# Performance work log

Hardware: AMD Instinct MI355X
Metric: run time of the kernel (lower is better)

The kernel has to match this reference:

```python
import jax, jax.numpy as jnp
import numpy as np

B, M, C, S, SD, K, H = 32, 448, 384, 512, 128, 8, 8
DH = C // H
EPS = 1e-5
NEG_SLOPE = 0.2


def setup_inputs() -> dict:
    key = jax.random.key(0)
    ks = iter(jax.random.split(key, 32))
    nrm = lambda shape, scale=0.05: (jax.random.normal(next(ks), shape, jnp.float32) * scale)
    inp = {
        'q': jax.random.normal(next(ks), (B, M, C), jnp.float32),
        'coarse': jax.random.normal(next(ks), (B, M, 3), jnp.float32),
        'skeleton': jax.random.normal(next(ks), (B, S, 3), jnp.float32),
        # GraphConv 1: 3 -> 64 (root weight, rel/neighbor weight, bias)
        'gc1_wroot': nrm((3, 64), 0.3), 'gc1_wrel': nrm((3, 64), 0.3), 'gc1_b': jnp.zeros((64,), jnp.float32),
        # GraphConv 2: 64 -> SD
        'gc2_wroot': nrm((64, SD), 0.1), 'gc2_wrel': nrm((64, SD), 0.1), 'gc2_b': jnp.zeros((SD,), jnp.float32),
        # skeleton_projection: SD -> C
        'proj_w': nrm((SD, C), 0.08), 'proj_b': jnp.zeros((C,), jnp.float32),
        # MultiheadAttention (torch layout: in_proj (3C, C), out_proj (C, C))
        'attn_in_w': nrm((3 * C, C), 0.05), 'attn_in_b': jnp.zeros((3 * C,), jnp.float32),
        'attn_out_w': nrm((C, C), 0.05), 'attn_out_b': jnp.zeros((C,), jnp.float32),
        # increase_dim: Conv1d(C,1024,1) + BN(1024) + LeakyReLU + Conv1d(1024,1024,1)
        'inc1_w': nrm((1024, C), 0.05), 'inc1_b': jnp.zeros((1024,), jnp.float32),
        'bn_g': jnp.ones((1024,), jnp.float32), 'bn_b': jnp.zeros((1024,), jnp.float32),
        'bn_m': jnp.zeros((1024,), jnp.float32), 'bn_v': jnp.ones((1024,), jnp.float32),
        'inc2_w': nrm((1024, 1024), 0.03), 'inc2_b': jnp.zeros((1024,), jnp.float32),
        # reduce_map: Linear(C + 1024 + 3, C)
        'red_w': nrm((1024 + C + 3, C), 0.03), 'red_b': jnp.zeros((C,), jnp.float32),
    }
    return inp


def _knn_idx(pts):
    # pts: [B,S,3]; per-batch kNN (self excluded), matching knn_graph(k=K, batch=...)
    d2 = jnp.sum((pts[:, :, None, :] - pts[:, None, :, :]) ** 2, axis=-1)  # [B,S,S]
    d2 = d2 + jnp.eye(S, dtype=pts.dtype)[None] * 1e10                       # mask self
    _, idx = jax.lax.top_k(-d2, K)                                           # [B,S,K]
    return idx


def _graph_conv(x, idx, wroot, wrel, b):
    # GraphConv (PyG, aggr='add'): out_i = x_i Wroot + (sum_{j in N(i)} x_j) Wrel + b
    nb = jax.vmap(lambda f, i: f[i])(x, idx)   # [B,S,K,F]
    agg = nb.sum(axis=2)                       # [B,S,F]
    return x @ wroot + agg @ wrel + b


def reference(q, coarse, skeleton, gc1_wroot, gc1_wrel, gc1_b, gc2_wroot, gc2_wrel, gc2_b,
              proj_w, proj_b, attn_in_w, attn_in_b, attn_out_w, attn_out_b,
              inc1_w, inc1_b, bn_g, bn_b, bn_m, bn_v, inc2_w, inc2_b, red_w, red_b):
    # --- skeleton branch: knn graph + 2-layer GraphConv + max-pool + projection ---
    idx = _knn_idx(skeleton)
    h = _graph_conv(skeleton, idx, gc1_wroot, gc1_wrel, gc1_b)
    h = jax.nn.relu(h)
    h = _graph_conv(h, idx, gc2_wroot, gc2_wrel, gc2_b)        # [B,S,SD]
    proxy = jnp.max(h, axis=1)                                  # [B,SD]
    proxy = proxy @ proj_w + proj_b                             # [B,C]
    kv = jnp.broadcast_to(proxy[:, None, :], (B, M, C))         # expanded proxies

    # --- cross attention (torch nn.MultiheadAttention math) ---
    wq, wk, wv = attn_in_w[:C], attn_in_w[C:2 * C], attn_in_w[2 * C:]
    bq, bk, bv = attn_in_b[:C], attn_in_b[C:2 * C], attn_in_b[2 * C:]
    qh = (q @ wq.T + bq).reshape(B, M, H, DH)
    kh = (kv @ wk.T + bk).reshape(B, M, H, DH)
    vh = (kv @ wv.T + bv).reshape(B, M, H, DH)
    scores = jnp.einsum('bmhd,bnhd->bhmn', qh, kh) / jnp.sqrt(jnp.float32(DH))
    attn = jax.nn.softmax(scores, axis=-1)
    ctx = jnp.einsum('bhmn,bnhd->bmhd', attn, vh).reshape(B, M, C)
    q = ctx @ attn_out_w.T + attn_out_b                         # fused features [B,M,C]

    # --- increase_dim (1x1 conv == matmul) + BN(eval) + LeakyReLU + 1x1 conv ---
    g = jnp.einsum('bmc,oc->bmo', q, inc1_w) + inc1_b           # [B,M,1024]
    g = bn_g * (g - bn_m) * jax.lax.rsqrt(bn_v + EPS) + bn_b
    g = jnp.where(g >= 0, g, NEG_SLOPE * g)
    g = jnp.einsum('bmc,oc->bmo', g, inc2_w) + inc2_b
    global_feature = jnp.max(g, axis=1)                         # [B,1024]

    # --- concat + reduce_map ---
    rebuild = jnp.concatenate([jnp.broadcast_to(global_feature[:, None, :], (B, M, 1024)), q, coarse], axis=-1)
    out = rebuild @ red_w + red_b                               # [B,M,C]
    return out
```

## Files before the change

kernel.cpp:

```cpp
#include <hip/hip_runtime.h>

#define NB 32
#define MM 448
#define CC 384
#define SS 512
#define KNN 8

#define WS_IDX   0u
#define WS_H1    524288u
#define WS_PMAX  (WS_H1 + 4194304u)
#define WS_Q     (WS_PMAX + 262144u)
#define WS_Y     (WS_Q + 49152u)
#define WS_G2    (WS_Y + 131072u)
#define WS_VV    WS_IDX

__global__ __launch_bounds__(256) void k_knn_gc1(
    const float* __restrict__ skel,
    const float* __restrict__ w1root, const float* __restrict__ w1rel,
    const float* __restrict__ b1,
    int* __restrict__ idx_ws, float* __restrict__ h1_ws)
{
  int b   = blockIdx.x >> 7;
  int grp = blockIdx.x & 127;
  __shared__ __align__(16) float4 sk[SS];
  const float* sb = skel + b * SS * 3;
  for (int t = threadIdx.x; t < SS; t += 256)
    sk[t] = make_float4(sb[t*3+0], sb[t*3+1], sb[t*3+2], 0.f);
  __syncthreads();

  int wave = threadIdx.x >> 6, lane = threadIdx.x & 63;
  int i = grp * 4 + wave;
  float4 pi = sk[i];

  float bd[KNN];
#pragma unroll
  for (int t = 0; t < KNN; t++) {
    int j = lane + (t << 6);
    float4 p = sk[j];
    float d2;
    {
#pragma clang fp contract(off)
      float dx = pi.x - p.x, dy = pi.y - p.y, dz = pi.z - p.z;
      d2 = (dx*dx + dy*dy) + dz*dz;
    }
    bd[t] = (j == i) ? 3e38f : d2;
  }

  int win[KNN];
  int* idx_base = idx_ws + (size_t)(b*SS + i) * KNN;
#pragma unroll
  for (int t = 0; t < KNN; t++) {
    float bestd = bd[0]; int bests = 0;
#pragma unroll
    for (int s = 1; s < KNN; s++)
      if (bd[s] < bestd) { bestd = bd[s]; bests = s; }
    int bestj = lane + (bests << 6);
#pragma unroll
    for (int m = 1; m < 64; m <<= 1) {
      float od = __shfl_xor(bestd, m, 64);
      int   oj = __shfl_xor(bestj, m, 64);
      if (od < bestd || (od == bestd && oj < bestj)) { bestd = od; bestj = oj; }
    }
    win[t] = bestj;
    if (lane == t) idx_base[t] = bestj;
    if ((bestj & 63) == lane) {
      int sl = bestj >> 6;
#pragma unroll
      for (int s = 0; s < KNN; s++) if (s == sl) bd[s] = 3e38f;
    }
  }

  float a0 = 0.f, a1 = 0.f, a2 = 0.f;
#pragma unroll
  for (int t = 0; t < KNN; t++) {
    float4 n = sk[win[t]];
    a0 += n.x; a1 += n.y; a2 += n.z;
  }

  int c = lane;
  float h = b1[c] + pi.x*w1root[c] + pi.y*w1root[64+c] + pi.z*w1root[128+c]
                  + a0*w1rel[c]   + a1*w1rel[64+c]   + a2*w1rel[128+c];
  h = fmaxf(h, 0.f);
  h1_ws[(size_t)(b*SS + i) * 64 + lane] = h;
}

__global__ __launch_bounds__(256) void k_gc2_max(
    const float* __restrict__ h1_ws, const int* __restrict__ idx_ws,
    const float* __restrict__ w2root, const float* __restrict__ w2rel,
    const float* __restrict__ b2, float* __restrict__ pmax)
{
  int b = blockIdx.x >> 4, chunk = blockIdx.x & 15;
  int r0 = chunk * 32;
  __shared__ __align__(16) float X[32*129];
  __shared__ __align__(16) float Wt[32*128];
  __shared__ float mred[8*128];
  __shared__ int nbs[32*KNN];

  const float* h1b = h1_ws + (size_t)b * SS * 64;
  nbs[threadIdx.x] = idx_ws[(b*SS + r0)*KNN + threadIdx.x];
#pragma unroll
  for (int p = 0; p < 8; p++) {
    int idx = threadIdx.x + 256*p;
    int r = idx >> 6, k = idx & 63;
    X[r*129 + k] = h1b[(r0 + r)*64 + k];
  }
  __syncthreads();
#pragma unroll
  for (int p = 0; p < 8; p++) {
    int idx = threadIdx.x + 256*p;
    int r = idx >> 6, k = idx & 63;
    const int* nb = nbs + r*KNN;
    float s = 0.f;
#pragma unroll
    for (int j = 0; j < KNN; j++) s += h1b[nb[j]*64 + k];
    X[r*129 + 64 + k] = s;
  }

  int rg = threadIdx.x >> 5, cg = threadIdx.x & 31;
  float acc[4][4];
#pragma unroll
  for (int r = 0; r < 4; r++)
#pragma unroll
    for (int u = 0; u < 4; u++) acc[r][u] = 0.f;

  const float* wsrc[4] = { w2root, w2root + 32*128, w2rel, w2rel + 32*128 };
#pragma unroll 1
  for (int ch = 0; ch < 4; ch++) {
    __syncthreads();
    const float* ws = wsrc[ch];
#pragma unroll
    for (int p = 0; p < 16; p++) {
      int idx = threadIdx.x + 256*p;
      Wt[idx] = ws[idx];
    }
    __syncthreads();
    int kb = ch * 32;
    const float* xr0 = X + (rg*4+0)*129 + kb;
    const float* xr1 = X + (rg*4+1)*129 + kb;
    const float* xr2 = X + (rg*4+2)*129 + kb;
    const float* xr3 = X + (rg*4+3)*129 + kb;
#pragma unroll 4
    for (int k = 0; k < 32; k++) {
      float4 w4 = *(const float4*)(Wt + k*128 + cg*4);
      float x0 = xr0[k], x1 = xr1[k], x2 = xr2[k], x3 = xr3[k];
      acc[0][0] += x0*w4.x; acc[0][1] += x0*w4.y; acc[0][2] += x0*w4.z; acc[0][3] += x0*w4.w;
      acc[1][0] += x1*w4.x; acc[1][1] += x1*w4.y; acc[1][2] += x1*w4.z; acc[1][3] += x1*w4.w;
      acc[2][0] += x2*w4.x; acc[2][1] += x2*w4.y; acc[2][2] += x2*w4.z; acc[2][3] += x2*w4.w;
      acc[3][0] += x3*w4.x; acc[3][1] += x3*w4.y; acc[3][2] += x3*w4.z; acc[3][3] += x3*w4.w;
    }
  }
#pragma unroll
  for (int u = 0; u < 4; u++)
    mred[rg*128 + cg*4 + u] =
      fmaxf(fmaxf(acc[0][u], acc[1][u]), fmaxf(acc[2][u], acc[3][u]));
  __syncthreads();
  if (threadIdx.x < 128) {
    int col = threadIdx.x;
    float mx = mred[col];
#pragma unroll
    for (int g = 1; g < 8; g++) mx = fmaxf(mx, mred[g*128 + col]);
    pmax[(size_t)(b*16 + chunk)*128 + col] = mx + b2[col];
  }
}

__global__ __launch_bounds__(256) void k_chainA(
    const float* __restrict__ pmax,
    const float* __restrict__ projw, const float* __restrict__ projb,
    const float* __restrict__ aiw, const float* __restrict__ aib,
    float* __restrict__ vv_ws)
{
  int b = blockIdx.x / 12, sl = blockIdx.x % 12;
  int t = threadIdx.x;
  __shared__ __align__(16) float proxy[128];
  __shared__ __align__(16) float kv[CC];
  if (t < 128) {
    float m = -3e38f;
    for (int ch = 0; ch < 16; ch++)
      m = fmaxf(m, pmax[(size_t)(b*16 + ch)*128 + t]);
    proxy[t] = m;
  }
  __syncthreads();
  for (int c = t; c < CC; c += 256) {
    float acc = projb[c];
    for (int s = 0; s < 128; s++) acc += proxy[s] * projw[s*CC + c];
    kv[c] = acc;
  }
  __syncthreads();
  int o = sl*32 + (t >> 3), qq = t & 7;
  const float* wr = aiw + (size_t)(2*CC + o) * CC + qq*48;
  const float* xr = kv + qq*48;
  float acc = 0.f;
#pragma unroll
  for (int k = 0; k < 48; k += 4) {
    float4 w4 = *(const float4*)(wr + k);
    float4 x4 = *(const float4*)(xr + k);
    acc += w4.x*x4.x + w4.y*x4.y + w4.z*x4.z + w4.w*x4.w;
  }
  acc += __shfl_xor(acc, 1, 64);
  acc += __shfl_xor(acc, 2, 64);
  acc += __shfl_xor(acc, 4, 64);
  if (qq == 0) vv_ws[b*CC + o] = acc + aib[2*CC + o];
}

__global__ __launch_bounds__(256) void k_chainB(
    const float* __restrict__ vv_ws,
    const float* __restrict__ aow, const float* __restrict__ aob,
    const float* __restrict__ i1w, const float* __restrict__ i1b,
    const float* __restrict__ bng, const float* __restrict__ bnb,
    const float* __restrict__ bnm, const float* __restrict__ bnv,
    float* __restrict__ q_ws, float* __restrict__ y_ws)
{
  int b = blockIdx.x >> 3, sl = blockIdx.x & 7;
  int t = threadIdx.x;
  __shared__ __align__(16) float vv[CC];
  __shared__ __align__(16) float qv[CC];
  for (int i = t; i < CC; i += 256) vv[i] = vv_ws[b*CC + i];
  __syncthreads();
  {
    int qq = t & 3;
    const float* xr = vv + qq*96;
#pragma unroll 1
    for (int r = 0; r < 6; r++) {
      int o = r*64 + (t >> 2);
      const float* wr = aow + (size_t)o * CC + qq*96;
      float acc = 0.f;
#pragma unroll
      for (int k = 0; k < 96; k += 4) {
        float4 w4 = *(const float4*)(wr + k);
        float4 x4 = *(const float4*)(xr + k);
        acc += w4.x*x4.x + w4.y*x4.y + w4.z*x4.z + w4.w*x4.w;
      }
      acc += __shfl_xor(acc, 1, 64);
      acc += __shfl_xor(acc, 2, 64);
      if (qq == 0) {
        float v = acc + aob[o];
        qv[o] = v;
        if (sl == 0) q_ws[b*CC + o] = v;
      }
    }
  }
  __syncthreads();
  {
    int o = sl*128 + (t >> 1), qq = t & 1;
    const float* wr = i1w + (size_t)o * CC + qq*192;
    const float* xr = qv + qq*192;
    float acc = 0.f;
#pragma unroll 12
    for (int k = 0; k < 192; k += 4) {
      float4 w4 = *(const float4*)(wr + k);
      float4 x4 = *(const float4*)(xr + k);
      acc += w4.x*x4.x + w4.y*x4.y + w4.z*x4.z + w4.w*x4.w;
    }
    acc += __shfl_xor(acc, 1, 64);
    if (qq == 0) {
      float a = acc + i1b[o];
      float z = bng[o] * (a - bnm[o]) * rsqrtf(bnv[o] + 1e-5f) + bnb[o];
      y_ws[b*1024 + o] = (z >= 0.f) ? z : 0.2f * z;
    }
  }
}

__global__ __launch_bounds__(256) void k_inc2(
    const float* __restrict__ y_ws, const float* __restrict__ inc2_w,
    const float* __restrict__ inc2_b, float* __restrict__ g2_ws)
{
  int b = blockIdx.x >> 4, og = blockIdx.x & 15;
  int t = threadIdx.x;
  int o = og*64 + (t >> 2), qq = t & 3;
  __shared__ __align__(16) float xs[1024];
  for (int i = t; i < 1024; i += 256) xs[i] = y_ws[b*1024 + i];
  __syncthreads();
  const float* wr = inc2_w + (size_t)o * 1024 + qq*256;
  const float* xr = xs + qq*256;
  float acc = 0.f;
#pragma unroll 8
  for (int kk = 0; kk < 256; kk += 4) {
    float4 w4 = *(const float4*)(wr + kk);
    float4 x4 = *(const float4*)(xr + kk);
    acc += w4.x*x4.x + w4.y*x4.y + w4.z*x4.z + w4.w*x4.w;
  }
  acc += __shfl_xor(acc, 1, 64);
  acc += __shfl_xor(acc, 2, 64);
  if (qq == 0) g2_ws[b*1024 + o] = acc + inc2_b[o];
}

__global__ __launch_bounds__(256) void k_base_out(
    const float* __restrict__ g2_ws, const float* __restrict__ q_ws,
    const float* __restrict__ red_w, const float* __restrict__ red_b,
    const float* __restrict__ coarse, float* __restrict__ out)
{
  int b = blockIdx.x;
  int o0 = blockIdx.y * 64;
  int wv = threadIdx.x >> 6, lane = threadIdx.x & 63;
  __shared__ __align__(16) float X[1408];
  __shared__ float part[4][64];
  __shared__ __align__(16) float baseS[64];
  for (int i = threadIdx.x; i < 1408; i += 256)
    X[i] = (i < 1024) ? g2_ws[b*1024 + i] : q_ws[b*CC + (i - 1024)];
  __syncthreads();
  int k0 = wv * 352;
  float acc = 0.f;
  const float* wbase = red_w + o0 + lane;
#pragma unroll 4
  for (int k = 0; k < 352; k++)
    acc += X[k0 + k] * wbase[(size_t)(k0 + k) * CC];
  part[wv][lane] = acc;
  __syncthreads();
  if (threadIdx.x < 64)
    baseS[lane] = part[0][lane] + part[1][lane] + part[2][lane] + part[3][lane]
                + red_b[o0 + lane];
  __syncthreads();
  int c4 = threadIdx.x & 15;
  int r0 = threadIdx.x >> 4;
  int c = o0 + c4*4;
  float4 base4 = *(const float4*)(baseS + c4*4);
  float4 w0 = *(const float4*)(red_w + (size_t)1408*CC + c);
  float4 w1 = *(const float4*)(red_w + (size_t)1409*CC + c);
  float4 w2 = *(const float4*)(red_w + (size_t)1410*CC + c);
#pragma unroll 4
  for (int m = r0; m < MM; m += 16) {
    const float* cr = coarse + (size_t)(b*MM + m) * 3;
    float cx = cr[0], cy = cr[1], cz = cr[2];
    float4 o4;
    o4.x = base4.x + cx*w0.x + cy*w1.x + cz*w2.x;
    o4.y = base4.y + cx*w0.y + cy*w1.y + cz*w2.y;
    o4.z = base4.z + cx*w0.z + cy*w1.z + cz*w2.z;
    o4.w = base4.w + cx*w0.w + cy*w1.w + cz*w2.w;
    *(float4*)(out + (size_t)(b*MM + m)*CC + c) = o4;
  }
}

extern "C" void kernel_launch(void* const* d_in, const int* in_sizes, int n_in,
                              void* d_out, int out_size, void* d_ws, size_t ws_size,
                              hipStream_t stream)
{
  (void)in_sizes; (void)n_in; (void)out_size; (void)ws_size;
  const float* coarse = (const float*)d_in[1];
  const float* skel   = (const float*)d_in[2];
  const float* g1wr   = (const float*)d_in[3];
  const float* g1wl   = (const float*)d_in[4];
  const float* g1b    = (const float*)d_in[5];
  const float* g2wr   = (const float*)d_in[6];
  const float* g2wl   = (const float*)d_in[7];
  const float* g2b    = (const float*)d_in[8];
  const float* projw  = (const float*)d_in[9];
  const float* projb  = (const float*)d_in[10];
  const float* aiw    = (const float*)d_in[11];
  const float* aib    = (const float*)d_in[12];
  const float* aow    = (const float*)d_in[13];
  const float* aob    = (const float*)d_in[14];
  const float* i1w    = (const float*)d_in[15];
  const float* i1b    = (const float*)d_in[16];
  const float* bng    = (const float*)d_in[17];
  const float* bnb    = (const float*)d_in[18];
  const float* bnm    = (const float*)d_in[19];
  const float* bnv    = (const float*)d_in[20];
  const float* i2w    = (const float*)d_in[21];
  const float* i2b    = (const float*)d_in[22];
  const float* redw   = (const float*)d_in[23];
  const float* redb   = (const float*)d_in[24];
  float* out = (float*)d_out;

  char* ws = (char*)d_ws;
  int*   idx_ws = (int*)(ws + WS_IDX);
  float* h1_ws  = (float*)(ws + WS_H1);
  float* pmax   = (float*)(ws + WS_PMAX);
  float* q_ws   = (float*)(ws + WS_Q);
  float* y_ws   = (float*)(ws + WS_Y);
  float* g2_ws  = (float*)(ws + WS_G2);
  float* vv_ws  = (float*)(ws + WS_VV);

  k_knn_gc1<<<4096, 256, 0, stream>>>(skel, g1wr, g1wl, g1b, idx_ws, h1_ws);
  k_gc2_max<<<512, 256, 0, stream>>>(h1_ws, idx_ws, g2wr, g2wl, g2b, pmax);
  k_chainA<<<384, 256, 0, stream>>>(pmax, projw, projb, aiw, aib, vv_ws);
  k_chainB<<<256, 256, 0, stream>>>(vv_ws, aow, aob, i1w, i1b,
                                    bng, bnb, bnm, bnv, q_ws, y_ws);
  k_inc2<<<512, 256, 0, stream>>>(y_ws, i2w, i2b, g2_ws);
  k_base_out<<<dim3(32, 6), 256, 0, stream>>>(g2_ws, q_ws, redw, redb, coarse, out);
}
```

Before: 267.7 us.

## Split reduce_map into batched split-K partial GEMV and parallel output broadcast

Replaces the single per-batch base/output kernel with two kernels. The first computes split-K partial products over 32-channel chunks for all 32 batches at once, so each red_w tile is loaded once and reused across batches instead of being reread per batch. The second sums the 44 partials, adds the bias and the coarse-coordinate term, and writes the output using a wider grid (32x14 blocks). This adds one kernel launch and a partial-sum buffer placed in the h1 workspace region.

```diff
diff --git a/kernel.cpp b/kernel.cpp
--- a/kernel.cpp
+++ b/kernel.cpp
@@ -12,6 +12,7 @@
 #define WS_Q     (WS_PMAX + 262144u)
 #define WS_Y     (WS_Q + 49152u)
 #define WS_G2    (WS_Y + 131072u)
+#define WS_PP    WS_H1
 #define WS_VV    WS_IDX
 
 __global__ __launch_bounds__(256) void k_knn_gc1(
@@ -284,49 +285,88 @@
   if (qq == 0) g2_ws[b*1024 + o] = acc + inc2_b[o];
 }
 
-__global__ __launch_bounds__(256) void k_base_out(
+__global__ __launch_bounds__(256) void k_basep(
     const float* __restrict__ g2_ws, const float* __restrict__ q_ws,
-    const float* __restrict__ red_w, const float* __restrict__ red_b,
-    const float* __restrict__ coarse, float* __restrict__ out)
-{
-  int b = blockIdx.x;
+    const float* __restrict__ red_w, float* __restrict__ pp)
+{
+  int cg = blockIdx.x;
   int o0 = blockIdx.y * 64;
-  int wv = threadIdx.x >> 6, lane = threadIdx.x & 63;
-  __shared__ __align__(16) float X[1408];
-  __shared__ float part[4][64];
-  __shared__ __align__(16) float baseS[64];
-  for (int i = threadIdx.x; i < 1408; i += 256)
-    X[i] = (i < 1024) ? g2_ws[b*1024 + i] : q_ws[b*CC + (i - 1024)];
-  __syncthreads();
-  int k0 = wv * 352;
-  float acc = 0.f;
-  const float* wbase = red_w + o0 + lane;
+  int c0 = cg * 32;
+  __shared__ __align__(16) float xs[32*33];
+  __shared__ __align__(16) float wt[32*64];
+#pragma unroll
+  for (int p = 0; p < 8; p++) {
+    int idx = threadIdx.x + 256*p;
+    int c = idx >> 6, o = idx & 63;
+    wt[idx] = red_w[(size_t)(c0 + c)*CC + o0 + o];
+  }
+  {
+    int b = threadIdx.x >> 3, cp = threadIdx.x & 7;
+    const float* src = (cg < 32) ? (g2_ws + b*1024 + c0)
+                                 : (q_ws  + b*CC   + (c0 - 1024));
+    float4 v = *(const float4*)(src + cp*4);
+    xs[(cp*4+0)*33 + b] = v.x;
+    xs[(cp*4+1)*33 + b] = v.y;
+    xs[(cp*4+2)*33 + b] = v.z;
+    xs[(cp*4+3)*33 + b] = v.w;
+  }
+  __syncthreads();
+  int b = threadIdx.x >> 3, og = threadIdx.x & 7;
+  float acc[8];
+#pragma unroll
+  for (int u = 0; u < 8; u++) acc[u] = 0.f;
+#pragma unroll 8
+  for (int c = 0; c < 32; c++) {
+    float xv = xs[c*33 + b];
+    float4 w0 = *(const float4*)(wt + c*64 + og*8);
+    float4 w1 = *(const float4*)(wt + c*64 + og*8 + 4);
+    acc[0] += xv*w0.x; acc[1] += xv*w0.y; acc[2] += xv*w0.z; acc[3] += xv*w0.w;
+    acc[4] += xv*w1.x; acc[5] += xv*w1.y; acc[6] += xv*w1.z; acc[7] += xv*w1.w;
+  }
+  float* dst = pp + (size_t)(cg*32 + b)*CC + o0 + og*8;
+  *(float4*)dst       = make_float4(acc[0], acc[1], acc[2], acc[3]);
+  *(float4*)(dst + 4) = make_float4(acc[4], acc[5], acc[6], acc[7]);
+}
+
+__global__ __launch_bounds__(256) void k_out2(
+    const float* __restrict__ pp, const float* __restrict__ red_b,
+    const float* __restrict__ red_w, const float* __restrict__ coarse,
+    float* __restrict__ out)
+{
+  int b = blockIdx.x, mc = blockIdx.y;
+  int t = threadIdx.x;
+  __shared__ __align__(16) float baseS[CC];
+  __shared__ __align__(16) float w3[3*CC];
+  __shared__ float crs[32*4];
+  for (int c = t; c < CC; c += 256) {
+    float s = red_b[c];
 #pragma unroll 4
-  for (int k = 0; k < 352; k++)
-    acc += X[k0 + k] * wbase[(size_t)(k0 + k) * CC];
-  part[wv][lane] = acc;
-  __syncthreads();
-  if (threadIdx.x < 64)
-    baseS[lane] = part[0][lane] + part[1][lane] + part[2][lane] + part[3][lane]
-                + red_b[o0 + lane];
-  __syncthreads();
-  int c4 = threadIdx.x & 15;
-  int r0 = threadIdx.x >> 4;
-  int c = o0 + c4*4;
-  float4 base4 = *(const float4*)(baseS + c4*4);
-  float4 w0 = *(const float4*)(red_w + (size_t)1408*CC + c);
-  float4 w1 = *(const float4*)(red_w + (size_t)1409*CC + c);
-  float4 w2 = *(const float4*)(red_w + (size_t)1410*CC + c);
+    for (int cg = 0; cg < 44; cg++) s += pp[(size_t)cg*12288 + b*CC + c];
+    baseS[c] = s;
+  }
+  for (int i = t; i < 3*CC; i += 256) w3[i] = red_w[(size_t)1408*CC + i];
+  if (t < 96) {
+    int r = t / 3, j = t % 3;
+    crs[r*4 + j] = coarse[(size_t)(b*MM + mc*32 + r)*3 + j];
+  }
+  __syncthreads();
+  int m0 = mc * 32;
 #pragma unroll 4
-  for (int m = r0; m < MM; m += 16) {
-    const float* cr = coarse + (size_t)(b*MM + m) * 3;
-    float cx = cr[0], cy = cr[1], cz = cr[2];
+  for (int p = 0; p < 12; p++) {
+    int idx = t + 256*p;
+    int r = idx / 96, c4 = idx % 96;
+    int c = c4 * 4;
+    float4 b4 = *(const float4*)(baseS + c);
+    float4 w0 = *(const float4*)(w3 + c);
+    float4 w1 = *(const float4*)(w3 + CC + c);
+    float4 w2 = *(const float4*)(w3 + 2*CC + c);
+    float cx = crs[r*4+0], cy = crs[r*4+1], cz = crs[r*4+2];
     float4 o4;
-    o4.x = base4.x + cx*w0.x + cy*w1.x + cz*w2.x;
-    o4.y = base4.y + cx*w0.y + cy*w1.y + cz*w2.y;
-    o4.z = base4.z + cx*w0.z + cy*w1.z + cz*w2.z;
-    o4.w = base4.w + cx*w0.w + cy*w1.w + cz*w2.w;
-    *(float4*)(out + (size_t)(b*MM + m)*CC + c) = o4;
+    o4.x = b4.x + cx*w0.x + cy*w1.x + cz*w2.x;
+    o4.y = b4.y + cx*w0.y + cy*w1.y + cz*w2.y;
+    o4.z = b4.z + cx*w0.z + cy*w1.z + cz*w2.z;
+    o4.w = b4.w + cx*w0.w + cy*w1.w + cz*w2.w;
+    *(float4*)(out + (size_t)(b*MM + m0 + r)*CC + c) = o4;
   }
 }
 
@@ -368,6 +408,7 @@
   float* q_ws   = (float*)(ws + WS_Q);
   float* y_ws   = (float*)(ws + WS_Y);
   float* g2_ws  = (float*)(ws + WS_G2);
+  float* pp     = (float*)(ws + WS_PP);
   float* vv_ws  = (float*)(ws + WS_VV);
 
   k_knn_gc1<<<4096, 256, 0, stream>>>(skel, g1wr, g1wl, g1b, idx_ws, h1_ws);
@@ -376,5 +417,6 @@
   k_chainB<<<256, 256, 0, stream>>>(vv_ws, aow, aob, i1w, i1b,
                                     bng, bnb, bnm, bnv, q_ws, y_ws);
   k_inc2<<<512, 256, 0, stream>>>(y_ws, i2w, i2b, g2_ws);
-  k_base_out<<<dim3(32, 6), 256, 0, stream>>>(g2_ws, q_ws, redw, redb, coarse, out);
-}
+  k_basep<<<dim3(44, 6), 256, 0, stream>>>(g2_ws, q_ws, redw, pp);
+  k_out2<<<dim3(32, 14), 256, 0, stream>>>(pp, redb, redw, coarse, out);
+}
```

New measurement: 247.1 us. -7.7%, faster.
